# Performance work log

Measured on AMD Instinct MI355X. Metric: run time of the kernel, lower is better.

## Reference

```python
import jax, jax.numpy as jnp
import numpy as np

S, B, IN, HID, DEPTH = 512, 64, 512, 512, 5
KEEP_IN = 1.0 - 0.75   # input_dropout = 0.75
KEEP_HID = 1.0 - 0.25  # hidden_dropout = 0.25


def _lin_init(k, shape, fan_in):
    bound = 1.0 / np.sqrt(fan_in)
    return jax.random.uniform(k, shape, jnp.float32, -bound, bound)


def setup_inputs() -> dict:
    key = jax.random.key(0)
    ks = jax.random.split(key, 14)
    inp = jax.random.normal(ks[0], (S, B, IN), jnp.float32)
    hidden = jax.random.normal(ks[1], (B, HID), jnp.float32)
    # tied_noise=True -> one input mask shared by H/T/C, one hidden mask shared
    h_mask = jax.random.bernoulli(ks[2], KEEP_IN, (B, IN)).astype(jnp.float32) / KEEP_IN
    s_h_mask = jax.random.bernoulli(ks[3], KEEP_HID, (B, HID)).astype(jnp.float32) / KEEP_HID
    # input projections (torch nn.Linear: W [out,in], y = x W^T + b)
    Wih = _lin_init(ks[4], (HID, IN), IN)
    bih = _lin_init(ks[5], (HID,), IN)
    Wit = _lin_init(ks[6], (HID, IN), IN)
    bit = _lin_init(ks[7], (HID,), IN)
    Wic = _lin_init(ks[8], (HID, IN), IN)
    bic = _lin_init(ks[9], (HID,), IN)
    # recurrent depth layers; layer 0 has no bias (set to 0)
    Wh = _lin_init(ks[10], (DEPTH, HID, HID), HID)
    bh = _lin_init(ks[11], (DEPTH, HID), HID).at[0].set(0.0)
    Wt = _lin_init(ks[12], (DEPTH, HID, HID), HID)
    bt = _lin_init(ks[13], (DEPTH, HID), HID).at[0].set(0.0)
    return dict(inp=inp, hidden=hidden, h_mask=h_mask, s_h_mask=s_h_mask,
                Wih=Wih, bih=bih, Wit=Wit, bit=bit, Wic=Wic, bic=bic,
                Wh=Wh, bh=bh, Wt=Wt, bt=bt)


def reference(inp, hidden, h_mask, s_h_mask, Wih, bih, Wit, bit, Wic, bic, Wh, bh, Wt, bt):
    # masked input (tied noise: same mask for H/T/C)
    mx = h_mask[None, :, :] * inp                      # [S,B,IN]
    H = jnp.einsum('sbi,hi->sbh', mx, Wih) + bih       # [S,B,HID]
    T = jnp.einsum('sbi,hi->sbh', mx, Wit) + bit
    C = jnp.einsum('sbi,hi->sbh', mx, Wic) + bic

    def step(s, htc):
        H_t, T_t, C_t = htc
        for l in range(DEPTH):
            sm = s_h_mask * s                          # [B,HID]
            lin_h = sm @ Wh[l].T + bh[l]
            lin_t = sm @ Wt[l].T + bt[l]               # NOTE: original uses rnn_t for C gate too
            if l == 0:
                h = jnp.tanh(H_t + lin_h)
                t = jax.nn.sigmoid(T_t + lin_t)
                c = jax.nn.sigmoid(C_t + lin_t)
            else:
                h = jnp.tanh(lin_h)
                t = jax.nn.sigmoid(lin_t)
                c = jax.nn.sigmoid(lin_t)
            s = h * t + s * c
        return s, s

    last, outs = jax.lax.scan(step, hidden, (H, T, C))
    return outs, last
```

## Files before the change

kernel.cpp:

```cpp
#include <hip/hip_runtime.h>
#include <math.h>

#define S_LEN 512
#define BATCH 64
#define IN_DIM 512
#define HID 512
#define DEPTH 5
#define N3 1536
#define NBLK 256

typedef float floatx4 __attribute__((ext_vector_type(4)));

#define STOREC(ptr, val) \
    asm volatile("global_store_dwordx4 %0, %1, off sc1" :: "v"(ptr), "v"(val) : "memory")

__global__ __launch_bounds__(256) void rhn_inproj(
    const float* __restrict__ inp, const float* __restrict__ h_mask,
    const float* __restrict__ Wih, const float* __restrict__ Wit,
    const float* __restrict__ Wic, const float* __restrict__ bih,
    const float* __restrict__ bit_, const float* __restrict__ bic,
    float* __restrict__ HTC)
{
    constexpr int BM = 128, BN = 128, BK = 16, LW = BM + 4;
    __shared__ float As[BK][LW];
    __shared__ float Bs[BK][LW];
    const int m0 = blockIdx.x * BM;
    const int n0 = blockIdx.y * BN;
    const int tid = threadIdx.x;
    const int lrow = tid & 127;
    const int lkq  = tid >> 7;
    const int tx = tid & 15, ty = tid >> 4;

    const float* Arow = inp + (size_t)(m0 + lrow) * 512;
    const float* Mrow = h_mask + (size_t)((m0 + lrow) & 63) * 512;
    const int n = n0 + lrow;
    const float* Wrow = (n < 512) ? (Wih + (size_t)n * 512)
                       : (n < 1024) ? (Wit + (size_t)(n - 512) * 512)
                                    : (Wic + (size_t)(n - 1024) * 512);

    float acc[8][8] = {};

    for (int k0 = 0; k0 < 512; k0 += BK) {
#pragma unroll
        for (int it = 0; it < 2; ++it) {
            int kq = lkq * 2 + it;
            float4 av = *(const float4*)(Arow + k0 + kq * 4);
            float4 mv = *(const float4*)(Mrow + k0 + kq * 4);
            float4 bv = *(const float4*)(Wrow + k0 + kq * 4);
            As[kq * 4 + 0][lrow] = av.x * mv.x;
            As[kq * 4 + 1][lrow] = av.y * mv.y;
            As[kq * 4 + 2][lrow] = av.z * mv.z;
            As[kq * 4 + 3][lrow] = av.w * mv.w;
            Bs[kq * 4 + 0][lrow] = bv.x;
            Bs[kq * 4 + 1][lrow] = bv.y;
            Bs[kq * 4 + 2][lrow] = bv.z;
            Bs[kq * 4 + 3][lrow] = bv.w;
        }
        __syncthreads();
#pragma unroll
        for (int kk = 0; kk < BK; ++kk) {
            float4 a0 = *(const float4*)&As[kk][ty * 8];
            float4 a1 = *(const float4*)&As[kk][ty * 8 + 4];
            float4 bv0 = *(const float4*)&Bs[kk][tx * 8];
            float4 bv1 = *(const float4*)&Bs[kk][tx * 8 + 4];
            float am[8] = {a0.x, a0.y, a0.z, a0.w, a1.x, a1.y, a1.z, a1.w};
            float bn[8] = {bv0.x, bv0.y, bv0.z, bv0.w, bv1.x, bv1.y, bv1.z, bv1.w};
#pragma unroll
            for (int i = 0; i < 8; ++i)
#pragma unroll
                for (int j = 0; j < 8; ++j)
                    acc[i][j] += am[i] * bn[j];
        }
        __syncthreads();
    }

    float bias[8];
#pragma unroll
    for (int j = 0; j < 8; ++j) {
        int nn = n0 + tx * 8 + j;
        bias[j] = (nn < 512) ? bih[nn] : (nn < 1024) ? bit_[nn - 512] : bic[nn - 1024];
    }
#pragma unroll
    for (int i = 0; i < 8; ++i) {
        int mm = m0 + ty * 8 + i;
        float4 o0, o1;
        o0.x = acc[i][0] + bias[0]; o0.y = acc[i][1] + bias[1];
        o0.z = acc[i][2] + bias[2]; o0.w = acc[i][3] + bias[3];
        o1.x = acc[i][4] + bias[4]; o1.y = acc[i][5] + bias[5];
        o1.z = acc[i][6] + bias[6]; o1.w = acc[i][7] + bias[7];
        *(float4*)(HTC + (size_t)mm * N3 + n0 + tx * 8)     = o0;
        *(float4*)(HTC + (size_t)mm * N3 + n0 + tx * 8 + 4) = o1;
    }
}

__device__ __forceinline__ float fast_sig(float x) {
    return __builtin_amdgcn_rcpf(1.f + __expf(-x));
}
__device__ __forceinline__ float fast_tanh(float x) {
    return 2.f * fast_sig(2.f * x) - 1.f;
}

__global__ __launch_bounds__(256) void rhn_scan(
    const float* __restrict__ hidden,
    const float* __restrict__ s_h_mask,
    const float* __restrict__ Wh, const float* __restrict__ bh,
    const float* __restrict__ Wt, const float* __restrict__ bt,
    const float* __restrict__ HTC,
    float* __restrict__ s_buf,
    float* __restrict__ out,
    unsigned* __restrict__ bar)
{
    constexpr int PAD = 4, LW = HID + PAD;
    __shared__ float mask_s[8][LW];
    __shared__ float sm_s[8][LW];
    __shared__ float linT[8][16];

    const int tid = threadIdx.x;
    const int hi = blockIdx.x & 31;
    const int bi = blockIdx.x >> 5;
    const int h0 = hi * 16, b0 = bi * 8;
    const int g   = tid >> 7;
    const int r   = tid & 127;
    const int hl2 = r >> 5;
    const int iq  = (r >> 3) & 3;
    const int bl  = r & 7;
    const int hbase = h0 + hl2 * 4;

    unsigned* ggen = bar + (size_t)bi * 32;
    unsigned* gcnt = bar + 256 + (size_t)bi * 32;

    const int p0 = tid,       b_0 = p0 >> 7, i40 = p0 & 127;
    const int p1 = tid + 256, b_1 = p1 >> 7, i41 = p1 & 127;
    const int p2 = tid + 512, b_2 = p2 >> 7, i42 = p2 & 127;
    const int p3 = tid + 768, b_3 = p3 >> 7, i43 = p3 & 127;

    *(float4*)&mask_s[b_0][i40 * 4] = ((const float4*)(s_h_mask + (size_t)(b0 + b_0) * HID))[i40];
    *(float4*)&mask_s[b_1][i41 * 4] = ((const float4*)(s_h_mask + (size_t)(b0 + b_1) * HID))[i41];
    *(float4*)&mask_s[b_2][i42 * 4] = ((const float4*)(s_h_mask + (size_t)(b0 + b_2) * HID))[i42];
    *(float4*)&mask_s[b_3][i43 * 4] = ((const float4*)(s_h_mask + (size_t)(b0 + b_3) * HID))[i43];

    const float* Wg = g ? Wt : Wh;
    const float* bg = g ? bt : bh;
    const bool tail = (g == 0 && iq == 0);

    floatx4 s_reg = {0, 0, 0, 0};
    float4 Hp = {0,0,0,0}, Tp = {0,0,0,0}, Cp = {0,0,0,0};
    if (tail) {
        float4 s0 = *(const float4*)(hidden + (size_t)(b0 + bl) * HID + hbase);
        s_reg.x = s0.x; s_reg.y = s0.y; s_reg.z = s0.z; s_reg.w = s0.w;
        const float* hp = HTC + (size_t)(b0 + bl) * N3 + hbase;
        Hp = *(const float4*)hp;
        Tp = *(const float4*)(hp + 512);
        Cp = *(const float4*)(hp + 1024);
    }

    const float* sp0 = s_buf + (size_t)(b0 + b_0) * HID + i40 * 4;
    const float* sp1 = s_buf + (size_t)(b0 + b_1) * HID + i41 * 4;
    const float* sp2 = s_buf + (size_t)(b0 + b_2) * HID + i42 * 4;
    const float* sp3 = s_buf + (size_t)(b0 + b_3) * HID + i43 * 4;

    int cur = 0;
    unsigned round = 0;
    bool pend_out = false;
    floatx4 pend_val = {0,0,0,0};

    for (int step = 0; step < S_LEN; ++step) {
        for (int l = 0; l < DEPTH; ++l) {
            const size_t coff = (size_t)cur * (BATCH * HID);

            if (pend_out) {
                *(float4*)(out + ((size_t)((step - (l == 0)) * BATCH + b0 + bl)) * HID + hbase)
                    = *(float4*)&pend_val;
                pend_out = false;
            }

            floatx4 sv0, sv1, sv2, sv3;
            asm volatile(
                "global_load_dwordx4 %0, %4, off sc1\n\t"
                "global_load_dwordx4 %1, %5, off sc1\n\t"
                "global_load_dwordx4 %2, %6, off sc1\n\t"
                "global_load_dwordx4 %3, %7, off sc1\n\t"
                "s_waitcnt vmcnt(0)"
                : "=&v"(sv0), "=&v"(sv1), "=&v"(sv2), "=&v"(sv3)
                : "v"(sp0 + coff), "v"(sp1 + coff), "v"(sp2 + coff), "v"(sp3 + coff)
                : "memory");
            {
                floatx4 m;
                m = *(const floatx4*)&mask_s[b_0][i40 * 4];
                *(floatx4*)&sm_s[b_0][i40 * 4] = sv0 * m;
                m = *(const floatx4*)&mask_s[b_1][i41 * 4];
                *(floatx4*)&sm_s[b_1][i41 * 4] = sv1 * m;
                m = *(const floatx4*)&mask_s[b_2][i42 * 4];
                *(floatx4*)&sm_s[b_2][i42 * 4] = sv2 * m;
                m = *(const floatx4*)&mask_s[b_3][i43 * 4];
                *(floatx4*)&sm_s[b_3][i43 * 4] = sv3 * m;
            }
            __syncthreads();

            const float* W0 = Wg + ((size_t)l * HID + hbase) * HID;
            const float* W1 = W0 + HID;
            const float* W2 = W0 + 2 * HID;
            const float* W3 = W0 + 3 * HID;
            float4 a0 = {0,0,0,0}, a1 = {0,0,0,0}, a2 = {0,0,0,0}, a3 = {0,0,0,0};
            const float4* smq = (const float4*)&sm_s[bl][0];
#pragma unroll 4
            for (int kk = 0; kk < 32; ++kk) {
                int i4 = iq * 32 + kk;
                float4 sv = smq[i4];
                float4 w0 = ((const float4*)W0)[i4];
                float4 w1 = ((const float4*)W1)[i4];
                float4 w2 = ((const float4*)W2)[i4];
                float4 w3 = ((const float4*)W3)[i4];
                a0.x += w0.x * sv.x; a0.y += w0.y * sv.y; a0.z += w0.z * sv.z; a0.w += w0.w * sv.w;
                a1.x += w1.x * sv.x; a1.y += w1.y * sv.y; a1.z += w1.z * sv.z; a1.w += w1.w * sv.w;
                a2.x += w2.x * sv.x; a2.y += w2.y * sv.y; a2.z += w2.z * sv.z; a2.w += w2.w * sv.w;
                a3.x += w3.x * sv.x; a3.y += w3.y * sv.y; a3.z += w3.z * sv.z; a3.w += w3.w * sv.w;
            }
            float lin[4];
            lin[0] = a0.x + a0.y + a0.z + a0.w;
            lin[1] = a1.x + a1.y + a1.z + a1.w;
            lin[2] = a2.x + a2.y + a2.z + a2.w;
            lin[3] = a3.x + a3.y + a3.z + a3.w;
#pragma unroll
            for (int j = 0; j < 4; ++j) {
                lin[j] += __shfl_xor(lin[j], 8);
                lin[j] += __shfl_xor(lin[j], 16);
                lin[j] += bg[l * HID + hbase + j];
            }
            if (g == 1 && iq == 0) {
                float4 o = {lin[0], lin[1], lin[2], lin[3]};
                *(float4*)&linT[bl][hl2 * 4] = o;
            }
            __syncthreads();

            if (tail) {
                float4 lt4 = *(const float4*)&linT[bl][hl2 * 4];
                float ltv[4] = {lt4.x, lt4.y, lt4.z, lt4.w};
                float sold[4] = {s_reg.x, s_reg.y, s_reg.z, s_reg.w};
                float Hv[4] = {Hp.x, Hp.y, Hp.z, Hp.w};
                float Tv[4] = {Tp.x, Tp.y, Tp.z, Tp.w};
                float Cv[4] = {Cp.x, Cp.y, Cp.z, Cp.w};
                float snew[4];
#pragma unroll
                for (int j = 0; j < 4; ++j) {
                    float lh = lin[j], lt = ltv[j];
                    float hv, tv, cv;
                    if (l == 0) {
                        hv = fast_tanh(Hv[j] + lh);
                        tv = fast_sig(Tv[j] + lt);
                        cv = fast_sig(Cv[j] + lt);
                    } else {
                        hv = fast_tanh(lh);
                        tv = fast_sig(lt);
                        cv = tv;
                    }
                    snew[j] = hv * tv + sold[j] * cv;
                }
                s_reg.x = snew[0]; s_reg.y = snew[1];
                s_reg.z = snew[2]; s_reg.w = snew[3];
                float* dp = s_buf + ((size_t)(cur ^ 1)) * (BATCH * HID)
                            + (size_t)(b0 + bl) * HID + hbase;
                STOREC(dp, s_reg);
                if (l == 0 && step + 1 < S_LEN) {
                    const float* hp = HTC + ((size_t)((step + 1) * BATCH + b0 + bl)) * N3 + hbase;
                    Hp = *(const float4*)hp;
                    Tp = *(const float4*)(hp + 512);
                    Cp = *(const float4*)(hp + 1024);
                }
                if (l == DEPTH - 1) {
                    pend_out = true;
                    pend_val = s_reg;
                }
            }
            cur ^= 1;

            asm volatile("s_waitcnt vmcnt(0)" ::: "memory");
            __syncthreads();
            if (tid == 0) {
                unsigned a = __hip_atomic_fetch_add(gcnt, 1u, __ATOMIC_RELAXED,
                                                    __HIP_MEMORY_SCOPE_AGENT);
                if (a == round * 32u + 31u) {
                    __hip_atomic_store(ggen, round + 1u, __ATOMIC_RELAXED,
                                       __HIP_MEMORY_SCOPE_AGENT);
                } else {
                    while (__hip_atomic_load(ggen, __ATOMIC_RELAXED,
                                             __HIP_MEMORY_SCOPE_AGENT) < round + 1u)
                        __builtin_amdgcn_s_sleep(1);
                }
            }
            __syncthreads();
            ++round;
        }
    }

    if (tail) {
        *(float4*)(out + ((size_t)((S_LEN - 1) * BATCH + b0 + bl)) * HID + hbase)
            = *(float4*)&pend_val;
        *(float4*)(out + (size_t)S_LEN * BATCH * HID + (size_t)(b0 + bl) * HID + hbase)
            = *(float4*)&pend_val;
    }
}

extern "C" void kernel_launch(void* const* d_in, const int* in_sizes, int n_in,
                              void* d_out, int out_size, void* d_ws, size_t ws_size,
                              hipStream_t stream) {
    const float* inp      = (const float*)d_in[0];
    const float* hidden   = (const float*)d_in[1];
    const float* h_mask   = (const float*)d_in[2];
    const float* s_h_mask = (const float*)d_in[3];
    const float* Wih = (const float*)d_in[4];
    const float* bih = (const float*)d_in[5];
    const float* Wit = (const float*)d_in[6];
    const float* bit_ = (const float*)d_in[7];
    const float* Wic = (const float*)d_in[8];
    const float* bic = (const float*)d_in[9];
    const float* Wh = (const float*)d_in[10];
    const float* bh = (const float*)d_in[11];
    const float* Wt = (const float*)d_in[12];
    const float* bt = (const float*)d_in[13];
    float* out = (float*)d_out;

    float* HTC   = (float*)d_ws;
    float* s_buf = HTC + (size_t)32768 * N3;
    unsigned* bar = (unsigned*)(s_buf + 2 * BATCH * HID);

    (void)hipMemsetAsync(bar, 0, 512 * sizeof(unsigned), stream);

    dim3 g1(256, 12);
    rhn_inproj<<<g1, 256, 0, stream>>>(inp, h_mask, Wih, Wit, Wic, bih, bit_, bic, HTC);

    (void)hipMemcpyAsync(s_buf, hidden, (size_t)BATCH * HID * sizeof(float),
                         hipMemcpyDeviceToDevice, stream);

    void* args[] = {(void*)&hidden, (void*)&s_h_mask, (void*)&Wh, (void*)&bh,
                    (void*)&Wt, (void*)&bt, (void*)&HTC, (void*)&s_buf,
                    (void*)&out, (void*)&bar};
    (void)hipLaunchCooperativeKernel((void*)rhn_scan, dim3(NBLK), dim3(256), args, 0, stream);
}
```

Baseline: 17.91 ms.

## Replace group barrier with tagged-value flag exchange and register-resident weights

```diff
diff --git a/kernel.cpp b/kernel.cpp
--- a/kernel.cpp
+++ b/kernel.cpp
@@ -7,12 +7,9 @@
 #define HID 512
 #define DEPTH 5
 #define N3 1536
-#define NBLK 256
 
 typedef float floatx4 __attribute__((ext_vector_type(4)));
-
-#define STOREC(ptr, val) \
-    asm volatile("global_store_dwordx4 %0, %1, off sc1" :: "v"(ptr), "v"(val) : "memory")
+typedef unsigned int uintx4 __attribute__((ext_vector_type(4)));
 
 __global__ __launch_bounds__(256) void rhn_inproj(
     const float* __restrict__ inp, const float* __restrict__ h_mask,
@@ -100,205 +97,167 @@
     return 2.f * fast_sig(2.f * x) - 1.f;
 }
 
-__global__ __launch_bounds__(256) void rhn_scan(
+__global__ __launch_bounds__(512, 2) void rhn_scan(
     const float* __restrict__ hidden,
     const float* __restrict__ s_h_mask,
     const float* __restrict__ Wh, const float* __restrict__ bh,
     const float* __restrict__ Wt, const float* __restrict__ bt,
     const float* __restrict__ HTC,
-    float* __restrict__ s_buf,
-    float* __restrict__ out,
-    unsigned* __restrict__ bar)
+    float* __restrict__ exch,
+    float* __restrict__ out)
 {
-    constexpr int PAD = 4, LW = HID + PAD;
-    __shared__ float mask_s[8][LW];
-    __shared__ float sm_s[8][LW];
-    __shared__ float linT[8][16];
-
-    const int tid = threadIdx.x;
-    const int hi = blockIdx.x & 31;
-    const int bi = blockIdx.x >> 5;
+    __shared__ float sm_s[8][HID];
+    __shared__ float linT[16][8];
+
+    const int tid  = threadIdx.x;
+    const int lane = tid & 63;
+    const int w    = tid >> 6;
+    const int c    = lane & 3;
+    const int kq   = (lane >> 2) & 15;
+    const int gh   = w * 4 + c;
+    const int g    = gh >> 4;
+    const int hl   = gh & 15;
+
+    const int hi = blockIdx.x >> 3;
+    const int bi = blockIdx.x & 7;
     const int h0 = hi * 16, b0 = bi * 8;
-    const int g   = tid >> 7;
-    const int r   = tid & 127;
-    const int hl2 = r >> 5;
-    const int iq  = (r >> 3) & 3;
-    const int bl  = r & 7;
-    const int hbase = h0 + hl2 * 4;
-
-    unsigned* ggen = bar + (size_t)bi * 32;
-    unsigned* gcnt = bar + 256 + (size_t)bi * 32;
-
-    const int p0 = tid,       b_0 = p0 >> 7, i40 = p0 & 127;
-    const int p1 = tid + 256, b_1 = p1 >> 7, i41 = p1 & 127;
-    const int p2 = tid + 512, b_2 = p2 >> 7, i42 = p2 & 127;
-    const int p3 = tid + 768, b_3 = p3 >> 7, i43 = p3 & 127;
-
-    *(float4*)&mask_s[b_0][i40 * 4] = ((const float4*)(s_h_mask + (size_t)(b0 + b_0) * HID))[i40];
-    *(float4*)&mask_s[b_1][i41 * 4] = ((const float4*)(s_h_mask + (size_t)(b0 + b_1) * HID))[i41];
-    *(float4*)&mask_s[b_2][i42 * 4] = ((const float4*)(s_h_mask + (size_t)(b0 + b_2) * HID))[i42];
-    *(float4*)&mask_s[b_3][i43 * 4] = ((const float4*)(s_h_mask + (size_t)(b0 + b_3) * HID))[i43];
-
-    const float* Wg = g ? Wt : Wh;
-    const float* bg = g ? bt : bh;
-    const bool tail = (g == 0 && iq == 0);
-
-    floatx4 s_reg = {0, 0, 0, 0};
-    float4 Hp = {0,0,0,0}, Tp = {0,0,0,0}, Cp = {0,0,0,0};
-    if (tail) {
-        float4 s0 = *(const float4*)(hidden + (size_t)(b0 + bl) * HID + hbase);
-        s_reg.x = s0.x; s_reg.y = s0.y; s_reg.z = s0.z; s_reg.w = s0.w;
-        const float* hp = HTC + (size_t)(b0 + bl) * N3 + hbase;
-        Hp = *(const float4*)hp;
-        Tp = *(const float4*)(hp + 512);
-        Cp = *(const float4*)(hp + 1024);
-    }
-
-    const float* sp0 = s_buf + (size_t)(b0 + b_0) * HID + i40 * 4;
-    const float* sp1 = s_buf + (size_t)(b0 + b_1) * HID + i41 * 4;
-    const float* sp2 = s_buf + (size_t)(b0 + b_2) * HID + i42 * 4;
-    const float* sp3 = s_buf + (size_t)(b0 + b_3) * HID + i43 * 4;
-
-    int cur = 0;
-    unsigned round = 0;
-    bool pend_out = false;
-    floatx4 pend_val = {0,0,0,0};
-
+
+    const int myb = ((kq & 1) << 2) | (kq & 2) | ((kq >> 2) & 1);
+    const bool own = (g == 0) && (kq < 8);
+    const bool lw  = (g == 1) && (kq < 8);
+
+    const float* Wsrc = g ? Wt : Wh;
+    float4 Wreg[DEPTH * 8];
+#pragma unroll
+    for (int l = 0; l < DEPTH; ++l)
+#pragma unroll
+        for (int j = 0; j < 8; ++j)
+            Wreg[l * 8 + j] = *(const float4*)(Wsrc
+                + ((size_t)l * HID + (h0 + hl)) * HID + (size_t)(j * 16 + kq) * 4);
+
+    float biasr[DEPTH];
+    const float* bsrc = g ? bt : bh;
+#pragma unroll
+    for (int l = 0; l < DEPTH; ++l) biasr[l] = bsrc[l * HID + h0 + hl];
+
+    const int pA = tid,       pB = tid + 512;
+    const int bA = pA >> 7,   kA = pA & 127;
+    const int bB = pB >> 7,   kB = pB & 127;
+    const size_t offA = ((size_t)(b0 + bA) * HID + (size_t)kA * 4) * sizeof(float);
+    const size_t offB = ((size_t)(b0 + bB) * HID + (size_t)kB * 4) * sizeof(float);
+    const size_t SLOT = (size_t)BATCH * HID * sizeof(float);
+
+    float s = 0.f, mymask = 0.f, Hp = 0.f, Tp = 0.f, Cp = 0.f;
+    size_t ownoff = 0;
+    if (own) {
+        const int gb = b0 + myb, hh = h0 + hl;
+        s      = hidden[(size_t)gb * HID + hh];
+        mymask = s_h_mask[(size_t)gb * HID + hh];
+        const float* hp = HTC + (size_t)gb * N3 + hh;
+        Hp = hp[0]; Tp = hp[512]; Cp = hp[1024];
+        ownoff = ((size_t)gb * HID + hh) * sizeof(float);
+        unsigned uu = (__float_as_uint(s * mymask) & ~7u);
+        char* p = (char*)exch + ownoff;
+        asm volatile("global_store_dword %0, %1, off sc1" :: "v"(p), "v"(uu) : "memory");
+    }
+
+    const float4* smq = (const float4*)&sm_s[0][0] + kq;
+
+    int seq = 0;
     for (int step = 0; step < S_LEN; ++step) {
-        for (int l = 0; l < DEPTH; ++l) {
-            const size_t coff = (size_t)cur * (BATCH * HID);
-
-            if (pend_out) {
-                *(float4*)(out + ((size_t)((step - (l == 0)) * BATCH + b0 + bl)) * HID + hbase)
-                    = *(float4*)&pend_val;
-                pend_out = false;
-            }
-
-            floatx4 sv0, sv1, sv2, sv3;
-            asm volatile(
-                "global_load_dwordx4 %0, %4, off sc1\n\t"
-                "global_load_dwordx4 %1, %5, off sc1\n\t"
-                "global_load_dwordx4 %2, %6, off sc1\n\t"
-                "global_load_dwordx4 %3, %7, off sc1\n\t"
-                "s_waitcnt vmcnt(0)"
-                : "=&v"(sv0), "=&v"(sv1), "=&v"(sv2), "=&v"(sv3)
-                : "v"(sp0 + coff), "v"(sp1 + coff), "v"(sp2 + coff), "v"(sp3 + coff)
-                : "memory");
-            {
-                floatx4 m;
-                m = *(const floatx4*)&mask_s[b_0][i40 * 4];
-                *(floatx4*)&sm_s[b_0][i40 * 4] = sv0 * m;
-                m = *(const floatx4*)&mask_s[b_1][i41 * 4];
-                *(floatx4*)&sm_s[b_1][i41 * 4] = sv1 * m;
-                m = *(const floatx4*)&mask_s[b_2][i42 * 4];
-                *(floatx4*)&sm_s[b_2][i42 * 4] = sv2 * m;
-                m = *(const floatx4*)&mask_s[b_3][i43 * 4];
-                *(floatx4*)&sm_s[b_3][i43 * 4] = sv3 * m;
-            }
-            __syncthreads();
-
-            const float* W0 = Wg + ((size_t)l * HID + hbase) * HID;
-            const float* W1 = W0 + HID;
-            const float* W2 = W0 + 2 * HID;
-            const float* W3 = W0 + 3 * HID;
-            float4 a0 = {0,0,0,0}, a1 = {0,0,0,0}, a2 = {0,0,0,0}, a3 = {0,0,0,0};
-            const float4* smq = (const float4*)&sm_s[bl][0];
-#pragma unroll 4
-            for (int kk = 0; kk < 32; ++kk) {
-                int i4 = iq * 32 + kk;
-                float4 sv = smq[i4];
-                float4 w0 = ((const float4*)W0)[i4];
-                float4 w1 = ((const float4*)W1)[i4];
-                float4 w2 = ((const float4*)W2)[i4];
-                float4 w3 = ((const float4*)W3)[i4];
-                a0.x += w0.x * sv.x; a0.y += w0.y * sv.y; a0.z += w0.z * sv.z; a0.w += w0.w * sv.w;
-                a1.x += w1.x * sv.x; a1.y += w1.y * sv.y; a1.z += w1.z * sv.z; a1.w += w1.w * sv.w;
-                a2.x += w2.x * sv.x; a2.y += w2.y * sv.y; a2.z += w2.z * sv.z; a2.w += w2.w * sv.w;
-                a3.x += w3.x * sv.x; a3.y += w3.y * sv.y; a3.z += w3.z * sv.z; a3.w += w3.w * sv.w;
-            }
-            float lin[4];
-            lin[0] = a0.x + a0.y + a0.z + a0.w;
-            lin[1] = a1.x + a1.y + a1.z + a1.w;
-            lin[2] = a2.x + a2.y + a2.z + a2.w;
-            lin[3] = a3.x + a3.y + a3.z + a3.w;
-#pragma unroll
-            for (int j = 0; j < 4; ++j) {
-                lin[j] += __shfl_xor(lin[j], 8);
-                lin[j] += __shfl_xor(lin[j], 16);
-                lin[j] += bg[l * HID + hbase + j];
-            }
-            if (g == 1 && iq == 0) {
-                float4 o = {lin[0], lin[1], lin[2], lin[3]};
-                *(float4*)&linT[bl][hl2 * 4] = o;
-            }
-            __syncthreads();
-
-            if (tail) {
-                float4 lt4 = *(const float4*)&linT[bl][hl2 * 4];
-                float ltv[4] = {lt4.x, lt4.y, lt4.z, lt4.w};
-                float sold[4] = {s_reg.x, s_reg.y, s_reg.z, s_reg.w};
-                float Hv[4] = {Hp.x, Hp.y, Hp.z, Hp.w};
-                float Tv[4] = {Tp.x, Tp.y, Tp.z, Tp.w};
-                float Cv[4] = {Cp.x, Cp.y, Cp.z, Cp.w};
-                float snew[4];
-#pragma unroll
-                for (int j = 0; j < 4; ++j) {
-                    float lh = lin[j], lt = ltv[j];
-                    float hv, tv, cv;
-                    if (l == 0) {
-                        hv = fast_tanh(Hv[j] + lh);
-                        tv = fast_sig(Tv[j] + lt);
-                        cv = fast_sig(Cv[j] + lt);
-                    } else {
-                        hv = fast_tanh(lh);
-                        tv = fast_sig(lt);
-                        cv = tv;
-                    }
-                    snew[j] = hv * tv + sold[j] * cv;
-                }
-                s_reg.x = snew[0]; s_reg.y = snew[1];
-                s_reg.z = snew[2]; s_reg.w = snew[3];
-                float* dp = s_buf + ((size_t)(cur ^ 1)) * (BATCH * HID)
-                            + (size_t)(b0 + bl) * HID + hbase;
-                STOREC(dp, s_reg);
-                if (l == 0 && step + 1 < S_LEN) {
-                    const float* hp = HTC + ((size_t)((step + 1) * BATCH + b0 + bl)) * N3 + hbase;
-                    Hp = *(const float4*)hp;
-                    Tp = *(const float4*)(hp + 512);
-                    Cp = *(const float4*)(hp + 1024);
-                }
-                if (l == DEPTH - 1) {
-                    pend_out = true;
-                    pend_val = s_reg;
-                }
-            }
-            cur ^= 1;
-
-            asm volatile("s_waitcnt vmcnt(0)" ::: "memory");
-            __syncthreads();
-            if (tid == 0) {
-                unsigned a = __hip_atomic_fetch_add(gcnt, 1u, __ATOMIC_RELAXED,
-                                                    __HIP_MEMORY_SCOPE_AGENT);
-                if (a == round * 32u + 31u) {
-                    __hip_atomic_store(ggen, round + 1u, __ATOMIC_RELAXED,
-                                       __HIP_MEMORY_SCOPE_AGENT);
-                } else {
-                    while (__hip_atomic_load(ggen, __ATOMIC_RELAXED,
-                                             __HIP_MEMORY_SCOPE_AGENT) < round + 1u)
-                        __builtin_amdgcn_s_sleep(1);
-                }
-            }
-            __syncthreads();
-            ++round;
+#define ROUND(L)                                                                  \
+        {                                                                         \
+            const unsigned tg = (unsigned)(seq & 7);                              \
+            const char* sb = (const char*)exch + (size_t)(seq & 1) * SLOT;        \
+            const char* pa = sb + offA;                                           \
+            const char* pb = sb + offB;                                           \
+            uintx4 ua, ub;                                                        \
+            for (;;) {                                                            \
+                asm volatile("global_load_dwordx4 %0, %2, off sc1\n\t"            \
+                             "global_load_dwordx4 %1, %3, off sc1\n\t"            \
+                             "s_waitcnt vmcnt(0)"                                 \
+                             : "=&v"(ua), "=&v"(ub)                               \
+                             : "v"(pa), "v"(pb) : "memory");                      \
+                unsigned mm = (ua.x ^ tg) | (ua.y ^ tg) | (ua.z ^ tg) | (ua.w ^ tg) \
+                            | (ub.x ^ tg) | (ub.y ^ tg) | (ub.z ^ tg) | (ub.w ^ tg); \
+                if ((mm & 7u) == 0u) break;                                       \
+            }                                                                     \
+            *(uintx4*)&sm_s[bA][kA * 4] = ua;                                     \
+            *(uintx4*)&sm_s[bB][kB * 4] = ub;                                     \
+            __syncthreads();                         \
+            float acc[8] = {0.f, 0.f, 0.f, 0.f, 0.f, 0.f, 0.f, 0.f};              \
+            _Pragma("unroll")                                                     \
+            for (int j = 0; j < 8; ++j) {                                         \
+                const float4 wv = Wreg[(L) * 8 + j];                              \
+                _Pragma("unroll")                                                 \
+                for (int b = 0; b < 8; ++b) {                                     \
+                    const float4 sv = smq[b * 128 + j * 16];                      \
+                    acc[b] = fmaf(wv.x, sv.x, acc[b]);                            \
+                    acc[b] = fmaf(wv.y, sv.y, acc[b]);                            \
+                    acc[b] = fmaf(wv.z, sv.z, acc[b]);                            \
+                    acc[b] = fmaf(wv.w, sv.w, acc[b]);                            \
+                }                                                                 \
+            }                                                                     \
+            {           \
+                const bool u0 = (lane & 4) != 0;                                  \
+                const bool u1 = (lane & 8) != 0;                                  \
+                const bool u2 = (lane & 16) != 0;                                 \
+                _Pragma("unroll")                                                 \
+                for (int i = 0; i < 4; ++i) {                                     \
+                    float snd = u0 ? acc[i] : acc[i + 4];                         \
+                    float kp  = u0 ? acc[i + 4] : acc[i];                         \
+                    acc[i] = kp + __shfl_xor(snd, 4);                             \
+                }                                                                 \
+                _Pragma("unroll")                                                 \
+                for (int i = 0; i < 2; ++i) {                                     \
+                    float snd = u1 ? acc[i] : acc[i + 2];                         \
+                    float kp  = u1 ? acc[i + 2] : acc[i];                         \
+                    acc[i] = kp + __shfl_xor(snd, 8);                             \
+                }                                                                 \
+                {                                                                 \
+                    float snd = u2 ? acc[0] : acc[1];                             \
+                    float kp  = u2 ? acc[1] : acc[0];                             \
+                    acc[0] = kp + __shfl_xor(snd, 16);                            \
+                }                                                                 \
+                acc[0] += __shfl_xor(acc[0], 32);                                 \
+            }                                                                     \
+            const float lin = acc[0] + biasr[L];                                  \
+            if (lw) linT[hl][myb] = lin;                                          \
+            __syncthreads();                \
+            if (own) {                                                            \
+                const float lt = linT[hl][myb];                                   \
+                float hv, tv, cv;                                                 \
+                if ((L) == 0) {                                                   \
+                    hv = fast_tanh(Hp + lin);                                     \
+                    tv = fast_sig(Tp + lt);                                       \
+                    cv = fast_sig(Cp + lt);                                       \
+                } else {                                                          \
+                    hv = fast_tanh(lin);                                          \
+                    tv = fast_sig(lt);                                            \
+                    cv = tv;                                                      \
+                }                                                                 \
+                s = hv * tv + s * cv;                                             \
+                unsigned uu = (__float_as_uint(s * mymask) & ~7u)                 \
+                            | (unsigned)((seq + 1) & 7);                          \
+                char* p = (char*)exch + (size_t)((seq + 1) & 1) * SLOT + ownoff;  \
+                asm volatile("global_store_dword %0, %1, off sc1"                 \
+                             :: "v"(p), "v"(uu) : "memory");                      \
+                if ((L) == 0 && step + 1 < S_LEN) {                               \
+                    const float* hp = HTC + ((size_t)(step + 1) * BATCH           \
+                                      + (b0 + myb)) * N3 + (h0 + hl);             \
+                    Hp = hp[0]; Tp = hp[512]; Cp = hp[1024];                      \
+                }                                                                 \
+                if ((L) == DEPTH - 1)                                             \
+                    out[((size_t)step * BATCH + (b0 + myb)) * HID + (h0 + hl)] = s; \
+            }                                                                     \
+            ++seq;                                                                \
         }
-    }
-
-    if (tail) {
-        *(float4*)(out + ((size_t)((S_LEN - 1) * BATCH + b0 + bl)) * HID + hbase)
-            = *(float4*)&pend_val;
-        *(float4*)(out + (size_t)S_LEN * BATCH * HID + (size_t)(b0 + bl) * HID + hbase)
-            = *(float4*)&pend_val;
-    }
+        ROUND(0) ROUND(1) ROUND(2) ROUND(3) ROUND(4)
+#undef ROUND
+    }
+
+    if (own)
+        out[(size_t)S_LEN * BATCH * HID + (size_t)(b0 + myb) * HID + (h0 + hl)] = s;
 }
 
 extern "C" void kernel_launch(void* const* d_in, const int* in_sizes, int n_in,
@@ -320,20 +279,15 @@
     const float* bt = (const float*)d_in[13];
     float* out = (float*)d_out;
 
-    float* HTC   = (float*)d_ws;
-    float* s_buf = HTC + (size_t)32768 * N3;
-    unsigned* bar = (unsigned*)(s_buf + 2 * BATCH * HID);
-
-    (void)hipMemsetAsync(bar, 0, 512 * sizeof(unsigned), stream);
+    float* HTC  = (float*)d_ws;
+    float* exch = HTC + (size_t)32768 * N3;
+
+    (void)hipMemsetAsync(exch, 0xFF, 2 * (size_t)BATCH * HID * sizeof(float), stream);
 
     dim3 g1(256, 12);
     rhn_inproj<<<g1, 256, 0, stream>>>(inp, h_mask, Wih, Wit, Wic, bih, bit_, bic, HTC);
 
-    (void)hipMemcpyAsync(s_buf, hidden, (size_t)BATCH * HID * sizeof(float),
-                         hipMemcpyDeviceToDevice, stream);
-
     void* args[] = {(void*)&hidden, (void*)&s_h_mask, (void*)&Wh, (void*)&bh,
-                    (void*)&Wt, (void*)&bt, (void*)&HTC, (void*)&s_buf,
-                    (void*)&out, (void*)&bar};
-    (void)hipLaunchCooperativeKernel((void*)rhn_scan, dim3(NBLK), dim3(256), args, 0, stream);
-}
+                    (void*)&Wt, (void*)&bt, (void*)&HTC, (void*)&exch, (void*)&out};
+    (void)hipLaunchCooperativeKernel((void*)rhn_scan, dim3(256), dim3(512), args, 0, stream);
+}
```

New measurement: 17.37 ms. -3.0%, faster.
